# Kernel tuning notes

Measured on AMD Instinct MI355X. Metric: run time of the kernel, lower is better.

The kernel has to match this reference:

```python
import jax, jax.numpy as jnp
import numpy as np

H = 1024   # hidden_size
I = 2048   # intermediate_size
E = 16     # num_experts
K = 2      # num_experts_per_tok
B, T = 2, 2048


def setup_inputs() -> dict:
    key = jax.random.key(0)
    k1, k2, k3, k4 = jax.random.split(key, 4)
    x = jax.random.normal(k1, (B, T, H), dtype=jnp.float32)
    # torch nn.Linear weight layout: [out_features, in_features]
    Wg = jax.random.normal(k2, (E, H), dtype=jnp.float32) * 0.02   # gate
    W1 = jax.random.normal(k3, (E, I, H), dtype=jnp.float32) * 0.02  # fc1 per expert
    W2 = jax.random.normal(k4, (E, H, I), dtype=jnp.float32) * 0.02  # fc2 per expert
    return {"x": x, "Wg": Wg, "W1": W1, "W2": W2}


def reference(x, Wg, W1, W2):
    Bq, Tq, Hq = x.shape
    nt = Bq * Tq
    x_flat = x.reshape(nt, Hq)                       # [nt, H]
    gate_logits = x_flat @ Wg.T                      # [nt, E]
    gate_probs = jax.nn.softmax(gate_logits, axis=-1)
    topk_vals, topk_idx = jax.lax.top_k(gate_probs, K)  # [nt, K]
    # dense combine weights: zero for unselected (token, expert) pairs
    rows = jnp.arange(nt)[:, None]                   # [nt, 1]
    cw = jnp.zeros((nt, E), dtype=x.dtype).at[rows, topk_idx].add(topk_vals)
    # per-expert dense SiLU-MLP; combine weight of 0 makes unselected
    # contributions exactly zero, matching the original gather/scatter math.
    y_flat = jnp.zeros_like(x_flat)
    for e in range(E):
        h = jax.nn.silu(x_flat @ W1[e].T)            # [nt, I]
        o = h @ W2[e].T                              # [nt, H]
        y_flat = y_flat + cw[:, e:e + 1] * o
    return y_flat.reshape(Bq, Tq, Hq)
```

## Files before the change

kernel.cpp:

```cpp
#include <hip/hip_runtime.h>
#include <hip/hip_bf16.h>

#define H_DIM 1024
#define I_DIM 2048
#define NEXP  16
#define NTOK  4096
#define BM 128
#define BN 128
#define BK 32
#define ABUF (BM*BK)
#define BBUF (BN*BK)
#define MAXS 10240
#define MAXRB (MAXS/BM)
#define NC1 (I_DIM/BN)
#define NC2 (H_DIM/BN)
#define PAIRS (NTOK*2)
#define SORT_T 256
#define PPT (PAIRS/SORT_T)

typedef __attribute__((ext_vector_type(8))) short short8;
typedef __attribute__((ext_vector_type(4))) short short4v;
typedef __attribute__((ext_vector_type(4))) float f32x4;

#define OFF_TOKE 256
#define OFF_TOKW (OFF_TOKE + PAIRS*4)
#define OFF_TOS  (OFF_TOKW + PAIRS*4)
#define OFF_WOS  (OFF_TOS + MAXS*4)
#define OFF_H    (OFF_WOS + MAXS*4)
#define OFF_XBF  (OFF_H + (size_t)MAXS*I_DIM*2)
#define NEED_XBF (OFF_XBF + (size_t)NTOK*H_DIM*2)

#define GLDS16(gsrc, ldst) \
  __builtin_amdgcn_global_load_lds((const __attribute__((address_space(1))) void*)(gsrc), \
                                   (__attribute__((address_space(3))) void*)(ldst), 16, 0, 0)

__device__ inline short f2bf(float f) {
    union { float f; unsigned u; } v; v.f = f;
    unsigned u = v.u + 0x7FFFu + ((v.u >> 16) & 1u);
    return (short)(u >> 16);
}

__device__ inline short8 pack8(const float4 a, const float4 b) {
    return (short8){ f2bf(a.x), f2bf(a.y), f2bf(a.z), f2bf(a.w),
                     f2bf(b.x), f2bf(b.y), f2bf(b.z), f2bf(b.w) };
}

__device__ inline int xcd_swz(int bid, int nwg) {
    return (bid & 7) * (nwg >> 3) + (bid >> 3);
}

template<bool WRITE_XBF>
__global__ __launch_bounds__(256) void gate_kernel(
    const float* __restrict__ x, const float* __restrict__ Wg,
    int* __restrict__ tokE, float* __restrict__ tokW, short* __restrict__ xbf)
{
    const int tok  = blockIdx.x * 4 + (threadIdx.x >> 6);
    const int lane = threadIdx.x & 63;
    const float4* xr = (const float4*)(x + (size_t)tok * H_DIM);

    float acc[NEXP];
#pragma unroll
    for (int e = 0; e < NEXP; e++) acc[e] = 0.f;
#pragma unroll
    for (int j = 0; j < H_DIM/4; j += 64) {
        const float4 xv = xr[j + lane];
        if constexpr (WRITE_XBF) {
            *(short4v*)(xbf + (size_t)tok * H_DIM + (j + lane) * 4) =
                (short4v){ f2bf(xv.x), f2bf(xv.y), f2bf(xv.z), f2bf(xv.w) };
        }
#pragma unroll
        for (int e = 0; e < NEXP; e++) {
            const float4 wv = ((const float4*)(Wg + e * H_DIM))[j + lane];
            acc[e] = fmaf(xv.x, wv.x, fmaf(xv.y, wv.y, fmaf(xv.z, wv.z, fmaf(xv.w, wv.w, acc[e]))));
        }
    }
#pragma unroll
    for (int off = 32; off; off >>= 1) {
#pragma unroll
        for (int e = 0; e < NEXP; e++) acc[e] += __shfl_xor(acc[e], off, 64);
    }
    if (lane == 0) {
        float m = acc[0];
#pragma unroll
        for (int e = 1; e < NEXP; e++) m = fmaxf(m, acc[e]);
        float p[NEXP]; float s = 0.f;
#pragma unroll
        for (int e = 0; e < NEXP; e++) { p[e] = __expf(acc[e] - m); s += p[e]; }
        int i1 = 0;
#pragma unroll
        for (int e = 1; e < NEXP; e++) if (acc[e] > acc[i1]) i1 = e;
        int i2 = -1;
#pragma unroll
        for (int e = 0; e < NEXP; e++) {
            if (e == i1) continue;
            if (i2 < 0 || acc[e] > acc[i2]) i2 = e;
        }
        const float inv = 1.f / s;
        tokE[tok*2+0] = i1; tokW[tok*2+0] = p[i1] * inv;
        tokE[tok*2+1] = i2; tokW[tok*2+1] = p[i2] * inv;
    }
}

__global__ __launch_bounds__(SORT_T) void sort_kernel(
    const int* __restrict__ tokE, const float* __restrict__ tokW,
    int* __restrict__ aoff, int* __restrict__ tok_of_slot, float* __restrict__ w_of_slot)
{
    __shared__ int hist[NEXP * SORT_T];
    __shared__ int tot[NEXP];
    __shared__ int aoff_l[NEXP + 1];

    const int tid = threadIdx.x;
    const int lane = tid & 63, wv = tid >> 6;

    int eloc[PPT];
#pragma unroll
    for (int i = 0; i < PPT; i++) eloc[i] = tokE[tid * PPT + i];

#pragma unroll
    for (int e = 0; e < NEXP; e++) hist[e * SORT_T + tid] = 0;
    __syncthreads();
#pragma unroll
    for (int i = 0; i < PPT; i++) hist[eloc[i] * SORT_T + tid]++;
    __syncthreads();

#pragma unroll
    for (int r = 0; r < 4; r++) {
        const int e = wv * 4 + r;
        const int base = e * SORT_T + lane * 4;
        int v0 = hist[base+0], v1 = hist[base+1], v2 = hist[base+2], v3 = hist[base+3];
        const int s = v0 + v1 + v2 + v3;
        int incl = s;
#pragma unroll
        for (int off = 1; off < 64; off <<= 1) {
            const int t = __shfl_up(incl, off, 64);
            if (lane >= off) incl += t;
        }
        int run = incl - s;
        hist[base+0] = run; run += v0;
        hist[base+1] = run; run += v1;
        hist[base+2] = run; run += v2;
        hist[base+3] = run;
        if (lane == 63) tot[e] = incl;
    }
    __syncthreads();

    if (tid == 0) {
        int acc = 0;
#pragma unroll
        for (int e = 0; e < NEXP; e++) {
            aoff_l[e] = acc; aoff[e] = acc;
            acc += ((tot[e] + BM - 1) / BM) * BM;
        }
        aoff_l[NEXP] = acc; aoff[NEXP] = acc;
    }
    __syncthreads();

#pragma unroll
    for (int i = 0; i < PPT; i++) {
        const int p = tid * PPT + i;
        const int e = eloc[i];
        const int idx = hist[e * SORT_T + tid]++;
        const int slot = aoff_l[e] + idx;
        tok_of_slot[slot] = p >> 1;
        w_of_slot[slot] = tokW[p];
    }
}

template<int AMODE>
__global__ __launch_bounds__(256) void fc1_kernel_t(
    const void* __restrict__ xsrc, const float* __restrict__ W1,
    const int* __restrict__ aoff, const int* __restrict__ tok_of_slot,
    short* __restrict__ h)
{
    const int wg = xcd_swz(blockIdx.x, NC1 * MAXRB);
    const int colb = wg % NC1, rowb = wg / NC1;
    const int total = aoff[NEXP];
    const int row0 = rowb * BM;
    if (row0 >= total) return;
    int e = 0;
    while (aoff[e+1] <= row0) e++;
    const int col0 = colb * BN;

    __shared__ short As[2*ABUF];
    __shared__ short Bs[2*BBUF];

    const int tid = threadIdx.x, wid = tid>>6, lane = tid&63;
    const int wr = wid>>1, wc = wid&1;
    const int srow = wid*32 + (lane>>2);
    const int skc  = (lane&3)*8;

    int t0 = tok_of_slot[row0 + srow];      if (t0 < 0) t0 = 0;
    int t1 = tok_of_slot[row0 + srow + 16]; if (t1 < 0) t1 = 0;

    const float* wf0 = W1 + (size_t)e * I_DIM * H_DIM + (size_t)(col0 + srow)      * H_DIM + skc;
    const float* wf1 = W1 + (size_t)e * I_DIM * H_DIM + (size_t)(col0 + srow + 16) * H_DIM + skc;

    const short *sa0=nullptr,*sa1=nullptr;
    const float *fa0=nullptr,*fa1=nullptr;
    if constexpr (AMODE == 0) {
        const short* xb = (const short*)xsrc;
        sa0 = xb + (size_t)t0 * H_DIM + skc;
        sa1 = xb + (size_t)t1 * H_DIM + skc;
    } else {
        const float* xf = (const float*)xsrc;
        fa0 = xf + (size_t)t0 * H_DIM + skc;
        fa1 = xf + (size_t)t1 * H_DIM + skc;
    }
    short* la0 = &As[(wid*2+0)*512];
    short* la1 = &As[(wid*2+1)*512];

    const int frow = lane & 15, fko = (lane>>4)*8;

    f32x4 acc[4][4];
#pragma unroll
    for (int m=0;m<4;m++)
#pragma unroll
        for (int n=0;n<4;n++) acc[m][n] = (f32x4){0.f,0.f,0.f,0.f};

    float4 b00 = *(const float4*)(wf0), b01 = *(const float4*)(wf0+4);
    float4 b10 = *(const float4*)(wf1), b11 = *(const float4*)(wf1+4);
    float4 a00, a01, a10, a11;
    if constexpr (AMODE == 0) {
        GLDS16(sa0, la0);
        GLDS16(sa1, la1);
    } else {
        a00 = *(const float4*)(fa0); a01 = *(const float4*)(fa0+4);
        a10 = *(const float4*)(fa1); a11 = *(const float4*)(fa1+4);
        *(short8*)&As[srow*32 + skc]      = pack8(a00, a01);
        *(short8*)&As[(srow+16)*32 + skc] = pack8(a10, a11);
    }
    *(short8*)&Bs[srow*32 + skc]      = pack8(b00, b01);
    *(short8*)&Bs[(srow+16)*32 + skc] = pack8(b10, b11);
    __syncthreads();

    const int NT = H_DIM / BK;
    int cur = 0;
    for (int t = 0; t < NT; ++t) {
        const int kn = (t+1)*BK;
        const bool more = (t+1 < NT);
        if (more) {
            if constexpr (AMODE == 0) {
                GLDS16(sa0 + kn, la0 + (cur^1)*ABUF);
                GLDS16(sa1 + kn, la1 + (cur^1)*ABUF);
            } else {
                a00 = *(const float4*)(fa0+kn); a01 = *(const float4*)(fa0+kn+4);
                a10 = *(const float4*)(fa1+kn); a11 = *(const float4*)(fa1+kn+4);
            }
            b00 = *(const float4*)(wf0+kn); b01 = *(const float4*)(wf0+kn+4);
            b10 = *(const float4*)(wf1+kn); b11 = *(const float4*)(wf1+kn+4);
        }

        short8 af[4], bfr[4];
#pragma unroll
        for (int m=0;m<4;m++) af[m]  = *(const short8*)&As[cur*ABUF + (wr*64 + m*16 + frow)*32 + fko];
#pragma unroll
        for (int n=0;n<4;n++) bfr[n] = *(const short8*)&Bs[cur*BBUF + (wc*64 + n*16 + frow)*32 + fko];
#pragma unroll
        for (int m=0;m<4;m++)
#pragma unroll
            for (int n=0;n<4;n++)
                acc[m][n] = __builtin_amdgcn_mfma_f32_16x16x32_bf16(af[m], bfr[n], acc[m][n], 0, 0, 0);

        if (more) {
            if constexpr (AMODE == 1) {
                *(short8*)&As[(cur^1)*ABUF + srow*32 + skc]      = pack8(a00, a01);
                *(short8*)&As[(cur^1)*ABUF + (srow+16)*32 + skc] = pack8(a10, a11);
            }
            *(short8*)&Bs[(cur^1)*BBUF + srow*32 + skc]      = pack8(b00, b01);
            *(short8*)&Bs[(cur^1)*BBUF + (srow+16)*32 + skc] = pack8(b10, b11);
        }
        __syncthreads();
        cur ^= 1;
    }

    const int mr0 = row0 + wr*64 + (lane>>4)*4;
    const int nc0 = col0 + wc*64 + (lane&15);
#pragma unroll
    for (int m=0;m<4;m++)
#pragma unroll
        for (int n=0;n<4;n++)
#pragma unroll
            for (int r=0;r<4;r++) {
                const float v = acc[m][n][r];
                const float sv = v / (1.f + __expf(-v));
                h[(size_t)(mr0 + m*16 + r) * I_DIM + nc0 + n*16] = f2bf(sv);
            }
}

__global__ __launch_bounds__(256) void fc2_kernel(
    const short* __restrict__ h, const float* __restrict__ W2,
    const int* __restrict__ aoff, const int* __restrict__ tok_of_slot,
    const float* __restrict__ w_of_slot, float* __restrict__ y)
{
    const int wg = xcd_swz(blockIdx.x, NC2 * MAXRB);
    const int colb = wg % NC2, rowb = wg / NC2;
    const int total = aoff[NEXP];
    const int row0 = rowb * BM;
    if (row0 >= total) return;
    int e = 0;
    while (aoff[e+1] <= row0) e++;
    const int col0 = colb * BN;

    __shared__ short As[2*ABUF];
    __shared__ short Bs[2*BBUF];

    const int tid = threadIdx.x, wid = tid>>6, lane = tid&63;
    const int wr = wid>>1, wc = wid&1;
    const int srow = wid*32 + (lane>>2);
    const int skc  = (lane&3)*8;

    const short* sa0 = h + (size_t)(row0 + srow)      * I_DIM + skc;
    const short* sa1 = h + (size_t)(row0 + srow + 16) * I_DIM + skc;

    const float* wf0 = W2 + (size_t)e * H_DIM * I_DIM + (size_t)(col0 + srow)      * I_DIM + skc;
    const float* wf1 = W2 + (size_t)e * H_DIM * I_DIM + (size_t)(col0 + srow + 16) * I_DIM + skc;

    short* la0 = &As[(wid*2+0)*512];
    short* la1 = &As[(wid*2+1)*512];

    const int frow = lane & 15, fko = (lane>>4)*8;

    f32x4 acc[4][4];
#pragma unroll
    for (int m=0;m<4;m++)
#pragma unroll
        for (int n=0;n<4;n++) acc[m][n] = (f32x4){0.f,0.f,0.f,0.f};

    float4 b00 = *(const float4*)(wf0), b01 = *(const float4*)(wf0+4);
    float4 b10 = *(const float4*)(wf1), b11 = *(const float4*)(wf1+4);
    GLDS16(sa0, la0);
    GLDS16(sa1, la1);
    *(short8*)&Bs[srow*32 + skc]      = pack8(b00, b01);
    *(short8*)&Bs[(srow+16)*32 + skc] = pack8(b10, b11);
    __syncthreads();

    const int NT = I_DIM / BK;
    int cur = 0;
    for (int t = 0; t < NT; ++t) {
        const int kn = (t+1)*BK;
        const bool more = (t+1 < NT);
        if (more) {
            GLDS16(sa0 + kn, la0 + (cur^1)*ABUF);
            GLDS16(sa1 + kn, la1 + (cur^1)*ABUF);
            b00 = *(const float4*)(wf0+kn); b01 = *(const float4*)(wf0+kn+4);
            b10 = *(const float4*)(wf1+kn); b11 = *(const float4*)(wf1+kn+4);
        }

        short8 af[4], bfr[4];
#pragma unroll
        for (int m=0;m<4;m++) af[m]  = *(const short8*)&As[cur*ABUF + (wr*64 + m*16 + frow)*32 + fko];
#pragma unroll
        for (int n=0;n<4;n++) bfr[n] = *(const short8*)&Bs[cur*BBUF + (wc*64 + n*16 + frow)*32 + fko];
#pragma unroll
        for (int m=0;m<4;m++)
#pragma unroll
            for (int n=0;n<4;n++)
                acc[m][n] = __builtin_amdgcn_mfma_f32_16x16x32_bf16(af[m], bfr[n], acc[m][n], 0, 0, 0);

        if (more) {
            *(short8*)&Bs[(cur^1)*BBUF + srow*32 + skc]      = pack8(b00, b01);
            *(short8*)&Bs[(cur^1)*BBUF + (srow+16)*32 + skc] = pack8(b10, b11);
        }
        __syncthreads();
        cur ^= 1;
    }

    const int mr0 = row0 + wr*64 + (lane>>4)*4;
    const int nc0 = col0 + wc*64 + (lane&15);
#pragma unroll
    for (int m=0;m<4;m++)
#pragma unroll
        for (int r=0;r<4;r++) {
            const int slot = mr0 + m*16 + r;
            const int tok = tok_of_slot[slot];
            if (tok < 0) continue;
            const float w = w_of_slot[slot];
#pragma unroll
            for (int n=0;n<4;n++)
                atomicAdd(&y[(size_t)tok * H_DIM + nc0 + n*16], w * acc[m][n][r]);
        }
}

extern "C" void kernel_launch(void* const* d_in, const int* in_sizes, int n_in,
                              void* d_out, int out_size, void* d_ws, size_t ws_size,
                              hipStream_t stream) {
    const float* x  = (const float*)d_in[0];
    const float* Wg = (const float*)d_in[1];
    const float* W1 = (const float*)d_in[2];
    const float* W2 = (const float*)d_in[3];
    float* y = (float*)d_out;

    char* ws = (char*)d_ws;
    int*   aoff        = (int*)  (ws + 128);
    int*   tokE        = (int*)  (ws + OFF_TOKE);
    float* tokW        = (float*)(ws + OFF_TOKW);
    int*   tok_of_slot = (int*)  (ws + OFF_TOS);
    float* w_of_slot   = (float*)(ws + OFF_WOS);
    short* h           = (short*)(ws + OFF_H);
    short* xbf         = (short*)(ws + OFF_XBF);

    const bool hasXbf = (ws_size >= NEED_XBF);

    hipMemsetAsync(tok_of_slot, 0xFF, MAXS*4, stream);
    hipMemsetAsync(y, 0, (size_t)out_size * 4, stream);

    if (hasXbf) {
        gate_kernel<true><<<NTOK/4, 256, 0, stream>>>(x, Wg, tokE, tokW, xbf);
        sort_kernel<<<1, SORT_T, 0, stream>>>(tokE, tokW, aoff, tok_of_slot, w_of_slot);
        fc1_kernel_t<0><<<NC1*MAXRB, 256, 0, stream>>>(xbf, W1, aoff, tok_of_slot, h);
    } else {
        gate_kernel<false><<<NTOK/4, 256, 0, stream>>>(x, Wg, tokE, tokW, nullptr);
        sort_kernel<<<1, SORT_T, 0, stream>>>(tokE, tokW, aoff, tok_of_slot, w_of_slot);
        fc1_kernel_t<1><<<NC1*MAXRB, 256, 0, stream>>>(x, W1, aoff, tok_of_slot, h);
    }
    fc2_kernel<<<NC2*MAXRB, 256, 0, stream>>>(h, W2, aoff, tok_of_slot, w_of_slot, y);
}
```

Before: 261.8 us.

## Prefetch two K-tiles ahead in registers and barrier without waiting on vmem

Replaces direct global-to-LDS loads and the per-iteration __syncthreads with a register-staged pipeline in both expert GEMM kernels. Two register sets hold tiles t+1 and t+2, so global loads run two K-steps ahead. A custom barrier waits only on lgkmcnt and not on vmcnt, so outstanding global loads are not drained at each barrier. This costs more VGPRs for the double register staging, which could lower occupancy, and activations now pass through registers instead of the async LDS path.

Result: slower. 285.2 us (+8.9%).

```diff
diff --git a/kernel.cpp b/kernel.cpp
--- a/kernel.cpp
+++ b/kernel.cpp
@@ -30,10 +30,6 @@
 #define OFF_XBF  (OFF_H + (size_t)MAXS*I_DIM*2)
 #define NEED_XBF (OFF_XBF + (size_t)NTOK*H_DIM*2)
 
-#define GLDS16(gsrc, ldst) \
-  __builtin_amdgcn_global_load_lds((const __attribute__((address_space(1))) void*)(gsrc), \
-                                   (__attribute__((address_space(3))) void*)(ldst), 16, 0, 0)
-
 __device__ inline short f2bf(float f) {
     union { float f; unsigned u; } v; v.f = f;
     unsigned u = v.u + 0x7FFFu + ((v.u >> 16) & 1u);
@@ -48,6 +44,13 @@
 __device__ inline int xcd_swz(int bid, int nwg) {
     return (bid & 7) * (nwg >> 3) + (bid >> 3);
 }
+
+#define BARRIER_NOVM()                                     \
+    __builtin_amdgcn_sched_barrier(0);                     \
+    asm volatile("s_waitcnt lgkmcnt(0)" ::: "memory");     \
+    __builtin_amdgcn_sched_barrier(0);                     \
+    __builtin_amdgcn_s_barrier();                          \
+    __builtin_amdgcn_sched_barrier(0);
 
 template<bool WRITE_XBF>
 __global__ __launch_bounds__(256) void gate_kernel(
@@ -165,6 +168,12 @@
         w_of_slot[slot] = tokW[p];
     }
 }
+
+struct TileRegs {
+    short8 a0, a1;
+    float4 fa00, fa01, fa10, fa11;
+    float4 b00, b01, b10, b11;
+};
 
 template<int AMODE>
 __global__ __launch_bounds__(256) void fc1_kernel_t(
@@ -206,8 +215,6 @@
         fa0 = xf + (size_t)t0 * H_DIM + skc;
         fa1 = xf + (size_t)t1 * H_DIM + skc;
     }
-    short* la0 = &As[(wid*2+0)*512];
-    short* la1 = &As[(wid*2+1)*512];
 
     const int frow = lane & 15, fko = (lane>>4)*8;
 
@@ -217,60 +224,64 @@
 #pragma unroll
         for (int n=0;n<4;n++) acc[m][n] = (f32x4){0.f,0.f,0.f,0.f};
 
-    float4 b00 = *(const float4*)(wf0), b01 = *(const float4*)(wf0+4);
-    float4 b10 = *(const float4*)(wf1), b11 = *(const float4*)(wf1+4);
-    float4 a00, a01, a10, a11;
-    if constexpr (AMODE == 0) {
-        GLDS16(sa0, la0);
-        GLDS16(sa1, la1);
-    } else {
-        a00 = *(const float4*)(fa0); a01 = *(const float4*)(fa0+4);
-        a10 = *(const float4*)(fa1); a11 = *(const float4*)(fa1+4);
-        *(short8*)&As[srow*32 + skc]      = pack8(a00, a01);
-        *(short8*)&As[(srow+16)*32 + skc] = pack8(a10, a11);
-    }
-    *(short8*)&Bs[srow*32 + skc]      = pack8(b00, b01);
-    *(short8*)&Bs[(srow+16)*32 + skc] = pack8(b10, b11);
-    __syncthreads();
-
+#define P_LOAD(S, k)                                                          \
+    {                                                                         \
+        if constexpr (AMODE == 0) {                                           \
+            S.a0 = *(const short8*)(sa0 + (k));                               \
+            S.a1 = *(const short8*)(sa1 + (k));                               \
+        } else {                                                              \
+            S.fa00 = *(const float4*)(fa0 + (k)); S.fa01 = *(const float4*)(fa0 + (k) + 4); \
+            S.fa10 = *(const float4*)(fa1 + (k)); S.fa11 = *(const float4*)(fa1 + (k) + 4); \
+        }                                                                     \
+        S.b00 = *(const float4*)(wf0 + (k)); S.b01 = *(const float4*)(wf0 + (k) + 4); \
+        S.b10 = *(const float4*)(wf1 + (k)); S.b11 = *(const float4*)(wf1 + (k) + 4); \
+    }
+
+#define P_WRITE(S, buf)                                                       \
+    {                                                                         \
+        if constexpr (AMODE == 0) {                                           \
+            *(short8*)&As[(buf)*ABUF + srow*32 + skc]      = S.a0;            \
+            *(short8*)&As[(buf)*ABUF + (srow+16)*32 + skc] = S.a1;            \
+        } else {                                                              \
+            *(short8*)&As[(buf)*ABUF + srow*32 + skc]      = pack8(S.fa00, S.fa01); \
+            *(short8*)&As[(buf)*ABUF + (srow+16)*32 + skc] = pack8(S.fa10, S.fa11); \
+        }                                                                     \
+        *(short8*)&Bs[(buf)*BBUF + srow*32 + skc]      = pack8(S.b00, S.b01); \
+        *(short8*)&Bs[(buf)*BBUF + (srow+16)*32 + skc] = pack8(S.b10, S.b11); \
+    }
+
+#define P_MFMA(buf)                                                           \
+    {                                                                         \
+        short8 af[4], bfr[4];                                                 \
+        _Pragma("unroll")                                                     \
+        for (int m=0;m<4;m++) af[m]  = *(const short8*)&As[(buf)*ABUF + (wr*64 + m*16 + frow)*32 + fko]; \
+        _Pragma("unroll")                                                     \
+        for (int n=0;n<4;n++) bfr[n] = *(const short8*)&Bs[(buf)*BBUF + (wc*64 + n*16 + frow)*32 + fko]; \
+        _Pragma("unroll")                                                     \
+        for (int m=0;m<4;m++)                                                 \
+            _Pragma("unroll")                                                 \
+            for (int n=0;n<4;n++)                                             \
+                acc[m][n] = __builtin_amdgcn_mfma_f32_16x16x32_bf16(af[m], bfr[n], acc[m][n], 0, 0, 0); \
+    }
+
+    TileRegs s0, s1;
     const int NT = H_DIM / BK;
-    int cur = 0;
-    for (int t = 0; t < NT; ++t) {
-        const int kn = (t+1)*BK;
-        const bool more = (t+1 < NT);
-        if (more) {
-            if constexpr (AMODE == 0) {
-                GLDS16(sa0 + kn, la0 + (cur^1)*ABUF);
-                GLDS16(sa1 + kn, la1 + (cur^1)*ABUF);
-            } else {
-                a00 = *(const float4*)(fa0+kn); a01 = *(const float4*)(fa0+kn+4);
-                a10 = *(const float4*)(fa1+kn); a11 = *(const float4*)(fa1+kn+4);
-            }
-            b00 = *(const float4*)(wf0+kn); b01 = *(const float4*)(wf0+kn+4);
-            b10 = *(const float4*)(wf1+kn); b11 = *(const float4*)(wf1+kn+4);
-        }
-
-        short8 af[4], bfr[4];
-#pragma unroll
-        for (int m=0;m<4;m++) af[m]  = *(const short8*)&As[cur*ABUF + (wr*64 + m*16 + frow)*32 + fko];
-#pragma unroll
-        for (int n=0;n<4;n++) bfr[n] = *(const short8*)&Bs[cur*BBUF + (wc*64 + n*16 + frow)*32 + fko];
-#pragma unroll
-        for (int m=0;m<4;m++)
-#pragma unroll
-            for (int n=0;n<4;n++)
-                acc[m][n] = __builtin_amdgcn_mfma_f32_16x16x32_bf16(af[m], bfr[n], acc[m][n], 0, 0, 0);
-
-        if (more) {
-            if constexpr (AMODE == 1) {
-                *(short8*)&As[(cur^1)*ABUF + srow*32 + skc]      = pack8(a00, a01);
-                *(short8*)&As[(cur^1)*ABUF + (srow+16)*32 + skc] = pack8(a10, a11);
-            }
-            *(short8*)&Bs[(cur^1)*BBUF + srow*32 + skc]      = pack8(b00, b01);
-            *(short8*)&Bs[(cur^1)*BBUF + (srow+16)*32 + skc] = pack8(b10, b11);
-        }
-        __syncthreads();
-        cur ^= 1;
+
+    P_LOAD(s0, 0);
+    P_WRITE(s0, 0);
+    P_LOAD(s1, BK);
+    BARRIER_NOVM();
+
+    for (int t = 0; t < NT; t += 2) {
+        if (t + 2 < NT) { P_LOAD(s0, (t+2)*BK); }
+        P_MFMA(0);
+        if (t + 1 < NT) { P_WRITE(s1, 1); }
+        BARRIER_NOVM();
+
+        if (t + 3 < NT) { P_LOAD(s1, (t+3)*BK); }
+        P_MFMA(1);
+        if (t + 2 < NT) { P_WRITE(s0, 0); }
+        BARRIER_NOVM();
     }
 
     const int mr0 = row0 + wr*64 + (lane>>4)*4;
@@ -285,6 +296,9 @@
                 const float sv = v / (1.f + __expf(-v));
                 h[(size_t)(mr0 + m*16 + r) * I_DIM + nc0 + n*16] = f2bf(sv);
             }
+#undef P_LOAD
+#undef P_WRITE
+#undef P_MFMA
 }
 
 __global__ __launch_bounds__(256) void fc2_kernel(
@@ -315,9 +329,6 @@
     const float* wf0 = W2 + (size_t)e * H_DIM * I_DIM + (size_t)(col0 + srow)      * I_DIM + skc;
     const float* wf1 = W2 + (size_t)e * H_DIM * I_DIM + (size_t)(col0 + srow + 16) * I_DIM + skc;
 
-    short* la0 = &As[(wid*2+0)*512];
-    short* la1 = &As[(wid*2+1)*512];
-
     const int frow = lane & 15, fko = (lane>>4)*8;
 
     f32x4 acc[4][4];
@@ -326,43 +337,54 @@
 #pragma unroll
         for (int n=0;n<4;n++) acc[m][n] = (f32x4){0.f,0.f,0.f,0.f};
 
-    float4 b00 = *(const float4*)(wf0), b01 = *(const float4*)(wf0+4);
-    float4 b10 = *(const float4*)(wf1), b11 = *(const float4*)(wf1+4);
-    GLDS16(sa0, la0);
-    GLDS16(sa1, la1);
-    *(short8*)&Bs[srow*32 + skc]      = pack8(b00, b01);
-    *(short8*)&Bs[(srow+16)*32 + skc] = pack8(b10, b11);
-    __syncthreads();
-
+#define P_LOAD(S, k)                                                          \
+    {                                                                         \
+        S.a0 = *(const short8*)(sa0 + (k));                                   \
+        S.a1 = *(const short8*)(sa1 + (k));                                   \
+        S.b00 = *(const float4*)(wf0 + (k)); S.b01 = *(const float4*)(wf0 + (k) + 4); \
+        S.b10 = *(const float4*)(wf1 + (k)); S.b11 = *(const float4*)(wf1 + (k) + 4); \
+    }
+
+#define P_WRITE(S, buf)                                                       \
+    {                                                                         \
+        *(short8*)&As[(buf)*ABUF + srow*32 + skc]      = S.a0;                \
+        *(short8*)&As[(buf)*ABUF + (srow+16)*32 + skc] = S.a1;                \
+        *(short8*)&Bs[(buf)*BBUF + srow*32 + skc]      = pack8(S.b00, S.b01); \
+        *(short8*)&Bs[(buf)*BBUF + (srow+16)*32 + skc] = pack8(S.b10, S.b11); \
+    }
+
+#define P_MFMA(buf)                                                           \
+    {                                                                         \
+        short8 af[4], bfr[4];                                                 \
+        _Pragma("unroll")                                                     \
+        for (int m=0;m<4;m++) af[m]  = *(const short8*)&As[(buf)*ABUF + (wr*64 + m*16 + frow)*32 + fko]; \
+        _Pragma("unroll")                                                     \
+        for (int n=0;n<4;n++) bfr[n] = *(const short8*)&Bs[(buf)*BBUF + (wc*64 + n*16 + frow)*32 + fko]; \
+        _Pragma("unroll")                                                     \
+        for (int m=0;m<4;m++)                                                 \
+            _Pragma("unroll")                                                 \
+            for (int n=0;n<4;n++)                                             \
+                acc[m][n] = __builtin_amdgcn_mfma_f32_16x16x32_bf16(af[m], bfr[n], acc[m][n], 0, 0, 0); \
+    }
+
+    TileRegs s0, s1;
     const int NT = I_DIM / BK;
-    int cur = 0;
-    for (int t = 0; t < NT; ++t) {
-        const int kn = (t+1)*BK;
-        const bool more = (t+1 < NT);
-        if (more) {
-            GLDS16(sa0 + kn, la0 + (cur^1)*ABUF);
-            GLDS16(sa1 + kn, la1 + (cur^1)*ABUF);
-            b00 = *(const float4*)(wf0+kn); b01 = *(const float4*)(wf0+kn+4);
-            b10 = *(const float4*)(wf1+kn); b11 = *(const float4*)(wf1+kn+4);
-        }
-
-        short8 af[4], bfr[4];
-#pragma unroll
-        for (int m=0;m<4;m++) af[m]  = *(const short8*)&As[cur*ABUF + (wr*64 + m*16 + frow)*32 + fko];
-#pragma unroll
-        for (int n=0;n<4;n++) bfr[n] = *(const short8*)&Bs[cur*BBUF + (wc*64 + n*16 + frow)*32 + fko];
-#pragma unroll
-        for (int m=0;m<4;m++)
-#pragma unroll
-            for (int n=0;n<4;n++)
-                acc[m][n] = __builtin_amdgcn_mfma_f32_16x16x32_bf16(af[m], bfr[n], acc[m][n], 0, 0, 0);
-
-        if (more) {
-            *(short8*)&Bs[(cur^1)*BBUF + srow*32 + skc]      = pack8(b00, b01);
-            *(short8*)&Bs[(cur^1)*BBUF + (srow+16)*32 + skc] = pack8(b10, b11);
-        }
-        __syncthreads();
-        cur ^= 1;
+
+    P_LOAD(s0, 0);
+    P_WRITE(s0, 0);
+    P_LOAD(s1, BK);
+    BARRIER_NOVM();
+
+    for (int t = 0; t < NT; t += 2) {
+        if (t + 2 < NT) { P_LOAD(s0, (t+2)*BK); }
+        P_MFMA(0);
+        if (t + 1 < NT) { P_WRITE(s1, 1); }
+        BARRIER_NOVM();
+
+        if (t + 3 < NT) { P_LOAD(s1, (t+3)*BK); }
+        P_MFMA(1);
+        if (t + 2 < NT) { P_WRITE(s0, 0); }
+        BARRIER_NOVM();
     }
 
     const int mr0 = row0 + wr*64 + (lane>>4)*4;
@@ -379,6 +401,9 @@
             for (int n=0;n<4;n++)
                 atomicAdd(&y[(size_t)tok * H_DIM + nc0 + n*16], w * acc[m][n][r]);
         }
+#undef P_LOAD
+#undef P_WRITE
+#undef P_MFMA
 }
 
 extern "C" void kernel_launch(void* const* d_in, const int* in_sizes, int n_in,
```

## Pre-convert W2 to bf16 inside fc1 launch and load fc2 B tiles via LDS DMA

Applied to the files above, without the earlier changes.

When the workspace is large enough, every fc1 workgroup first runs a grid-stride loop that converts the full fp32 W2 tensor to bf16 in workspace. fc2 then streams bf16 W2 tiles straight into LDS with global_load_lds instead of loading fp32 and packing in registers. The fc2 main loop also drops double buffering for a single-buffer load/sync/compute/sync scheme. This halves fc2's weight read bytes and removes per-tile conversion, but adds a full W2 read and write pass each call and loses load/compute overlap in fc2.

New measurement: 264.7 us. Within noise of the previous version (+1.1%).

```diff
diff --git a/kernel.cpp b/kernel.cpp
--- a/kernel.cpp
+++ b/kernel.cpp
@@ -28,7 +28,9 @@
 #define OFF_WOS  (OFF_TOS + MAXS*4)
 #define OFF_H    (OFF_WOS + MAXS*4)
 #define OFF_XBF  (OFF_H + (size_t)MAXS*I_DIM*2)
-#define NEED_XBF (OFF_XBF + (size_t)NTOK*H_DIM*2)
+#define OFF_WBF  (OFF_XBF + (size_t)NTOK*H_DIM*2)
+#define NEED_XBF OFF_WBF
+#define NEED_FULL (OFF_WBF + (size_t)NEXP*I_DIM*H_DIM*2)
 
 #define GLDS16(gsrc, ldst) \
   __builtin_amdgcn_global_load_lds((const __attribute__((address_space(1))) void*)(gsrc), \
@@ -166,12 +168,23 @@
     }
 }
 
-template<int AMODE>
+template<int AMODE, bool CONVW2>
 __global__ __launch_bounds__(256) void fc1_kernel_t(
     const void* __restrict__ xsrc, const float* __restrict__ W1,
     const int* __restrict__ aoff, const int* __restrict__ tok_of_slot,
-    short* __restrict__ h)
+    short* __restrict__ h, const float* __restrict__ w2src, short* __restrict__ w2dst)
 {
+    if constexpr (CONVW2) {
+        const int n8 = NEXP*H_DIM*I_DIM/8;
+        int i = blockIdx.x * 256 + threadIdx.x;
+        const int stride = NC1*MAXRB*256;
+        for (; i < n8; i += stride) {
+            const float4 f0 = ((const float4*)w2src)[2*i];
+            const float4 f1 = ((const float4*)w2src)[2*i+1];
+            ((short8*)w2dst)[i] = pack8(f0, f1);
+        }
+    }
+
     const int wg = xcd_swz(blockIdx.x, NC1 * MAXRB);
     const int colb = wg % NC1, rowb = wg / NC1;
     const int total = aoff[NEXP];
@@ -287,8 +300,9 @@
             }
 }
 
-__global__ __launch_bounds__(256) void fc2_kernel(
-    const short* __restrict__ h, const float* __restrict__ W2,
+template<int MODE>
+__global__ __launch_bounds__(256) void fc2_kernel_t(
+    const short* __restrict__ h, const void* __restrict__ w2src,
     const int* __restrict__ aoff, const int* __restrict__ tok_of_slot,
     const float* __restrict__ w_of_slot, float* __restrict__ y)
 {
@@ -301,8 +315,8 @@
     while (aoff[e+1] <= row0) e++;
     const int col0 = colb * BN;
 
-    __shared__ short As[2*ABUF];
-    __shared__ short Bs[2*BBUF];
+    __shared__ short As[ABUF];
+    __shared__ short Bs[BBUF];
 
     const int tid = threadIdx.x, wid = tid>>6, lane = tid&63;
     const int wr = wid>>1, wc = wid&1;
@@ -312,11 +326,21 @@
     const short* sa0 = h + (size_t)(row0 + srow)      * I_DIM + skc;
     const short* sa1 = h + (size_t)(row0 + srow + 16) * I_DIM + skc;
 
-    const float* wf0 = W2 + (size_t)e * H_DIM * I_DIM + (size_t)(col0 + srow)      * I_DIM + skc;
-    const float* wf1 = W2 + (size_t)e * H_DIM * I_DIM + (size_t)(col0 + srow + 16) * I_DIM + skc;
-
+    const short *sb0=nullptr,*sb1=nullptr;
+    const float *fb0=nullptr,*fb1=nullptr;
+    if constexpr (MODE == 0) {
+        const short* wb = (const short*)w2src + (size_t)e * H_DIM * I_DIM;
+        sb0 = wb + (size_t)(col0 + srow)      * I_DIM + skc;
+        sb1 = wb + (size_t)(col0 + srow + 16) * I_DIM + skc;
+    } else {
+        const float* wf = (const float*)w2src + (size_t)e * H_DIM * I_DIM;
+        fb0 = wf + (size_t)(col0 + srow)      * I_DIM + skc;
+        fb1 = wf + (size_t)(col0 + srow + 16) * I_DIM + skc;
+    }
     short* la0 = &As[(wid*2+0)*512];
     short* la1 = &As[(wid*2+1)*512];
+    short* lb0 = &Bs[(wid*2+0)*512];
+    short* lb1 = &Bs[(wid*2+1)*512];
 
     const int frow = lane & 15, fko = (lane>>4)*8;
 
@@ -326,43 +350,31 @@
 #pragma unroll
         for (int n=0;n<4;n++) acc[m][n] = (f32x4){0.f,0.f,0.f,0.f};
 
-    float4 b00 = *(const float4*)(wf0), b01 = *(const float4*)(wf0+4);
-    float4 b10 = *(const float4*)(wf1), b11 = *(const float4*)(wf1+4);
-    GLDS16(sa0, la0);
-    GLDS16(sa1, la1);
-    *(short8*)&Bs[srow*32 + skc]      = pack8(b00, b01);
-    *(short8*)&Bs[(srow+16)*32 + skc] = pack8(b10, b11);
-    __syncthreads();
-
-    const int NT = I_DIM / BK;
-    int cur = 0;
-    for (int t = 0; t < NT; ++t) {
-        const int kn = (t+1)*BK;
-        const bool more = (t+1 < NT);
-        if (more) {
-            GLDS16(sa0 + kn, la0 + (cur^1)*ABUF);
-            GLDS16(sa1 + kn, la1 + (cur^1)*ABUF);
-            b00 = *(const float4*)(wf0+kn); b01 = *(const float4*)(wf0+kn+4);
-            b10 = *(const float4*)(wf1+kn); b11 = *(const float4*)(wf1+kn+4);
-        }
+    for (int k0 = 0; k0 < I_DIM; k0 += BK) {
+        GLDS16(sa0 + k0, la0);
+        GLDS16(sa1 + k0, la1);
+        if constexpr (MODE == 0) {
+            GLDS16(sb0 + k0, lb0);
+            GLDS16(sb1 + k0, lb1);
+        } else {
+            const float4 b00 = *(const float4*)(fb0 + k0), b01 = *(const float4*)(fb0 + k0 + 4);
+            const float4 b10 = *(const float4*)(fb1 + k0), b11 = *(const float4*)(fb1 + k0 + 4);
+            *(short8*)&Bs[srow*32 + skc]      = pack8(b00, b01);
+            *(short8*)&Bs[(srow+16)*32 + skc] = pack8(b10, b11);
+        }
+        __syncthreads();
 
         short8 af[4], bfr[4];
 #pragma unroll
-        for (int m=0;m<4;m++) af[m]  = *(const short8*)&As[cur*ABUF + (wr*64 + m*16 + frow)*32 + fko];
-#pragma unroll
-        for (int n=0;n<4;n++) bfr[n] = *(const short8*)&Bs[cur*BBUF + (wc*64 + n*16 + frow)*32 + fko];
+        for (int m=0;m<4;m++) af[m]  = *(const short8*)&As[(wr*64 + m*16 + frow)*32 + fko];
+#pragma unroll
+        for (int n=0;n<4;n++) bfr[n] = *(const short8*)&Bs[(wc*64 + n*16 + frow)*32 + fko];
 #pragma unroll
         for (int m=0;m<4;m++)
 #pragma unroll
             for (int n=0;n<4;n++)
                 acc[m][n] = __builtin_amdgcn_mfma_f32_16x16x32_bf16(af[m], bfr[n], acc[m][n], 0, 0, 0);
-
-        if (more) {
-            *(short8*)&Bs[(cur^1)*BBUF + srow*32 + skc]      = pack8(b00, b01);
-            *(short8*)&Bs[(cur^1)*BBUF + (srow+16)*32 + skc] = pack8(b10, b11);
-        }
         __syncthreads();
-        cur ^= 1;
     }
 
     const int mr0 = row0 + wr*64 + (lane>>4)*4;
@@ -398,20 +410,28 @@
     float* w_of_slot   = (float*)(ws + OFF_WOS);
     short* h           = (short*)(ws + OFF_H);
     short* xbf         = (short*)(ws + OFF_XBF);
-
+    short* wbf         = (short*)(ws + OFF_WBF);
+
+    const bool full   = (ws_size >= NEED_FULL);
     const bool hasXbf = (ws_size >= NEED_XBF);
 
     hipMemsetAsync(tok_of_slot, 0xFF, MAXS*4, stream);
     hipMemsetAsync(y, 0, (size_t)out_size * 4, stream);
 
-    if (hasXbf) {
+    if (full) {
         gate_kernel<true><<<NTOK/4, 256, 0, stream>>>(x, Wg, tokE, tokW, xbf);
         sort_kernel<<<1, SORT_T, 0, stream>>>(tokE, tokW, aoff, tok_of_slot, w_of_slot);
-        fc1_kernel_t<0><<<NC1*MAXRB, 256, 0, stream>>>(xbf, W1, aoff, tok_of_slot, h);
+        fc1_kernel_t<0, true><<<NC1*MAXRB, 256, 0, stream>>>(xbf, W1, aoff, tok_of_slot, h, W2, wbf);
+        fc2_kernel_t<0><<<NC2*MAXRB, 256, 0, stream>>>(h, wbf, aoff, tok_of_slot, w_of_slot, y);
+    } else if (hasXbf) {
+        gate_kernel<true><<<NTOK/4, 256, 0, stream>>>(x, Wg, tokE, tokW, xbf);
+        sort_kernel<<<1, SORT_T, 0, stream>>>(tokE, tokW, aoff, tok_of_slot, w_of_slot);
+        fc1_kernel_t<0, false><<<NC1*MAXRB, 256, 0, stream>>>(xbf, W1, aoff, tok_of_slot, h, nullptr, nullptr);
+        fc2_kernel_t<1><<<NC2*MAXRB, 256, 0, stream>>>(h, W2, aoff, tok_of_slot, w_of_slot, y);
     } else {
         gate_kernel<false><<<NTOK/4, 256, 0, stream>>>(x, Wg, tokE, tokW, nullptr);
         sort_kernel<<<1, SORT_T, 0, stream>>>(tokE, tokW, aoff, tok_of_slot, w_of_slot);
-        fc1_kernel_t<1><<<NC1*MAXRB, 256, 0, stream>>>(x, W1, aoff, tok_of_slot, h);
-    }
-    fc2_kernel<<<NC2*MAXRB, 256, 0, stream>>>(h, W2, aoff, tok_of_slot, w_of_slot, y);
-}
+        fc1_kernel_t<1, false><<<NC1*MAXRB, 256, 0, stream>>>(x, W1, aoff, tok_of_slot, h, nullptr, nullptr);
+        fc2_kernel_t<1><<<NC2*MAXRB, 256, 0, stream>>>(h, W2, aoff, tok_of_slot, w_of_slot, y);
+    }
+}
```

## Stage fp32 weights into LDS via direct loads with XOR swizzle, convert at fragment read

Applied to the files above, without the earlier changes.

Both expert GEMM kernels now copy the fp32 weight tiles straight from global memory into LDS with global_load_lds, using an XOR-swizzled column layout. Each thread converts to bf16 with v_cvt_pk_bf16_f32 when it reads its MFMA fragment, so the register staging and software f2bf packing of the B operand go away. The double-buffered pipeline is replaced by a single buffer with a sync before and after compute, so load latency is no longer overlapped with MFMA work. The B tile in LDS doubles in size because it is held as fp32.

After: 264.6 us. No clear change (+1.1%).

```diff
diff --git a/kernel.cpp b/kernel.cpp
--- a/kernel.cpp
+++ b/kernel.cpp
@@ -9,7 +9,7 @@
 #define BN 128
 #define BK 32
 #define ABUF (BM*BK)
-#define BBUF (BN*BK)
+#define BFL  (BN*BK)
 #define MAXS 10240
 #define MAXRB (MAXS/BM)
 #define NC1 (I_DIM/BN)
@@ -47,6 +47,19 @@
 
 __device__ inline int xcd_swz(int bid, int nwg) {
     return (bid & 7) * (nwg >> 3) + (bid >> 3);
+}
+
+__device__ inline short8 ldB(const float* Bs, int row, int l16) {
+    const int s  = (row & 7) * 16;
+    const char* base = (const char*)(Bs + row * 32);
+    const f32x4 lo = *(const f32x4*)(base + (((l16 * 32)      ) ^ s));
+    const f32x4 hi = *(const f32x4*)(base + (((l16 * 32) + 16 ) ^ s));
+    union { unsigned u[4]; short8 sv; } pk;
+    asm("v_cvt_pk_bf16_f32 %0, %1, %2" : "=v"(pk.u[0]) : "v"(lo[0]), "v"(lo[1]));
+    asm("v_cvt_pk_bf16_f32 %0, %1, %2" : "=v"(pk.u[1]) : "v"(lo[2]), "v"(lo[3]));
+    asm("v_cvt_pk_bf16_f32 %0, %1, %2" : "=v"(pk.u[2]) : "v"(hi[0]), "v"(hi[1]));
+    asm("v_cvt_pk_bf16_f32 %0, %1, %2" : "=v"(pk.u[3]) : "v"(hi[2]), "v"(hi[3]));
+    return pk.sv;
 }
 
 template<bool WRITE_XBF>
@@ -181,8 +194,8 @@
     while (aoff[e+1] <= row0) e++;
     const int col0 = colb * BN;
 
-    __shared__ short As[2*ABUF];
-    __shared__ short Bs[2*BBUF];
+    __shared__ short As[ABUF];
+    __shared__ __align__(16) float Bs[BFL];
 
     const int tid = threadIdx.x, wid = tid>>6, lane = tid&63;
     const int wr = wid>>1, wc = wid&1;
@@ -191,9 +204,6 @@
 
     int t0 = tok_of_slot[row0 + srow];      if (t0 < 0) t0 = 0;
     int t1 = tok_of_slot[row0 + srow + 16]; if (t1 < 0) t1 = 0;
-
-    const float* wf0 = W1 + (size_t)e * I_DIM * H_DIM + (size_t)(col0 + srow)      * H_DIM + skc;
-    const float* wf1 = W1 + (size_t)e * I_DIM * H_DIM + (size_t)(col0 + srow + 16) * H_DIM + skc;
 
     const short *sa0=nullptr,*sa1=nullptr;
     const float *fa0=nullptr,*fa1=nullptr;
@@ -209,7 +219,19 @@
     short* la0 = &As[(wid*2+0)*512];
     short* la1 = &As[(wid*2+1)*512];
 
-    const int frow = lane & 15, fko = (lane>>4)*8;
+    const float* Wb = W1 + (size_t)e * I_DIM * H_DIM;
+    const int br  = lane >> 3;
+    const int bco = ((lane & 7) ^ br) * 4;
+    const float* bs0 = Wb + (size_t)(col0 + (wid*4+0)*8 + br) * H_DIM + bco;
+    const float* bs1 = Wb + (size_t)(col0 + (wid*4+1)*8 + br) * H_DIM + bco;
+    const float* bs2 = Wb + (size_t)(col0 + (wid*4+2)*8 + br) * H_DIM + bco;
+    const float* bs3 = Wb + (size_t)(col0 + (wid*4+3)*8 + br) * H_DIM + bco;
+    float* lb0 = &Bs[(wid*4+0)*256];
+    float* lb1 = &Bs[(wid*4+1)*256];
+    float* lb2 = &Bs[(wid*4+2)*256];
+    float* lb3 = &Bs[(wid*4+3)*256];
+
+    const int frow = lane & 15, fko = (lane>>4)*8, l16 = lane>>4;
 
     f32x4 acc[4][4];
 #pragma unroll
@@ -217,60 +239,33 @@
 #pragma unroll
         for (int n=0;n<4;n++) acc[m][n] = (f32x4){0.f,0.f,0.f,0.f};
 
-    float4 b00 = *(const float4*)(wf0), b01 = *(const float4*)(wf0+4);
-    float4 b10 = *(const float4*)(wf1), b11 = *(const float4*)(wf1+4);
-    float4 a00, a01, a10, a11;
-    if constexpr (AMODE == 0) {
-        GLDS16(sa0, la0);
-        GLDS16(sa1, la1);
-    } else {
-        a00 = *(const float4*)(fa0); a01 = *(const float4*)(fa0+4);
-        a10 = *(const float4*)(fa1); a11 = *(const float4*)(fa1+4);
-        *(short8*)&As[srow*32 + skc]      = pack8(a00, a01);
-        *(short8*)&As[(srow+16)*32 + skc] = pack8(a10, a11);
-    }
-    *(short8*)&Bs[srow*32 + skc]      = pack8(b00, b01);
-    *(short8*)&Bs[(srow+16)*32 + skc] = pack8(b10, b11);
-    __syncthreads();
-
-    const int NT = H_DIM / BK;
-    int cur = 0;
-    for (int t = 0; t < NT; ++t) {
-        const int kn = (t+1)*BK;
-        const bool more = (t+1 < NT);
-        if (more) {
-            if constexpr (AMODE == 0) {
-                GLDS16(sa0 + kn, la0 + (cur^1)*ABUF);
-                GLDS16(sa1 + kn, la1 + (cur^1)*ABUF);
-            } else {
-                a00 = *(const float4*)(fa0+kn); a01 = *(const float4*)(fa0+kn+4);
-                a10 = *(const float4*)(fa1+kn); a11 = *(const float4*)(fa1+kn+4);
-            }
-            b00 = *(const float4*)(wf0+kn); b01 = *(const float4*)(wf0+kn+4);
-            b10 = *(const float4*)(wf1+kn); b11 = *(const float4*)(wf1+kn+4);
-        }
+    for (int k0 = 0; k0 < H_DIM; k0 += BK) {
+        if constexpr (AMODE == 0) {
+            GLDS16(sa0 + k0, la0);
+            GLDS16(sa1 + k0, la1);
+        } else {
+            const float4 a00 = *(const float4*)(fa0+k0), a01 = *(const float4*)(fa0+k0+4);
+            const float4 a10 = *(const float4*)(fa1+k0), a11 = *(const float4*)(fa1+k0+4);
+            *(short8*)&As[srow*32 + skc]      = pack8(a00, a01);
+            *(short8*)&As[(srow+16)*32 + skc] = pack8(a10, a11);
+        }
+        GLDS16(bs0 + k0, lb0);
+        GLDS16(bs1 + k0, lb1);
+        GLDS16(bs2 + k0, lb2);
+        GLDS16(bs3 + k0, lb3);
+        __syncthreads();
 
         short8 af[4], bfr[4];
 #pragma unroll
-        for (int m=0;m<4;m++) af[m]  = *(const short8*)&As[cur*ABUF + (wr*64 + m*16 + frow)*32 + fko];
-#pragma unroll
-        for (int n=0;n<4;n++) bfr[n] = *(const short8*)&Bs[cur*BBUF + (wc*64 + n*16 + frow)*32 + fko];
+        for (int m=0;m<4;m++) af[m]  = *(const short8*)&As[(wr*64 + m*16 + frow)*32 + fko];
+#pragma unroll
+        for (int n=0;n<4;n++) bfr[n] = ldB(Bs, wc*64 + n*16 + frow, l16);
 #pragma unroll
         for (int m=0;m<4;m++)
 #pragma unroll
             for (int n=0;n<4;n++)
                 acc[m][n] = __builtin_amdgcn_mfma_f32_16x16x32_bf16(af[m], bfr[n], acc[m][n], 0, 0, 0);
-
-        if (more) {
-            if constexpr (AMODE == 1) {
-                *(short8*)&As[(cur^1)*ABUF + srow*32 + skc]      = pack8(a00, a01);
-                *(short8*)&As[(cur^1)*ABUF + (srow+16)*32 + skc] = pack8(a10, a11);
-            }
-            *(short8*)&Bs[(cur^1)*BBUF + srow*32 + skc]      = pack8(b00, b01);
-            *(short8*)&Bs[(cur^1)*BBUF + (srow+16)*32 + skc] = pack8(b10, b11);
-        }
         __syncthreads();
-        cur ^= 1;
     }
 
     const int mr0 = row0 + wr*64 + (lane>>4)*4;
@@ -301,8 +296,8 @@
     while (aoff[e+1] <= row0) e++;
     const int col0 = colb * BN;
 
-    __shared__ short As[2*ABUF];
-    __shared__ short Bs[2*BBUF];
+    __shared__ short As[ABUF];
+    __shared__ __align__(16) float Bs[BFL];
 
     const int tid = threadIdx.x, wid = tid>>6, lane = tid&63;
     const int wr = wid>>1, wc = wid&1;
@@ -311,14 +306,22 @@
 
     const short* sa0 = h + (size_t)(row0 + srow)      * I_DIM + skc;
     const short* sa1 = h + (size_t)(row0 + srow + 16) * I_DIM + skc;
-
-    const float* wf0 = W2 + (size_t)e * H_DIM * I_DIM + (size_t)(col0 + srow)      * I_DIM + skc;
-    const float* wf1 = W2 + (size_t)e * H_DIM * I_DIM + (size_t)(col0 + srow + 16) * I_DIM + skc;
-
     short* la0 = &As[(wid*2+0)*512];
     short* la1 = &As[(wid*2+1)*512];
 
-    const int frow = lane & 15, fko = (lane>>4)*8;
+    const float* Wb = W2 + (size_t)e * H_DIM * I_DIM;
+    const int br  = lane >> 3;
+    const int bco = ((lane & 7) ^ br) * 4;
+    const float* bs0 = Wb + (size_t)(col0 + (wid*4+0)*8 + br) * I_DIM + bco;
+    const float* bs1 = Wb + (size_t)(col0 + (wid*4+1)*8 + br) * I_DIM + bco;
+    const float* bs2 = Wb + (size_t)(col0 + (wid*4+2)*8 + br) * I_DIM + bco;
+    const float* bs3 = Wb + (size_t)(col0 + (wid*4+3)*8 + br) * I_DIM + bco;
+    float* lb0 = &Bs[(wid*4+0)*256];
+    float* lb1 = &Bs[(wid*4+1)*256];
+    float* lb2 = &Bs[(wid*4+2)*256];
+    float* lb3 = &Bs[(wid*4+3)*256];
+
+    const int frow = lane & 15, fko = (lane>>4)*8, l16 = lane>>4;
 
     f32x4 acc[4][4];
 #pragma unroll
@@ -326,43 +329,26 @@
 #pragma unroll
         for (int n=0;n<4;n++) acc[m][n] = (f32x4){0.f,0.f,0.f,0.f};
 
-    float4 b00 = *(const float4*)(wf0), b01 = *(const float4*)(wf0+4);
-    float4 b10 = *(const float4*)(wf1), b11 = *(const float4*)(wf1+4);
-    GLDS16(sa0, la0);
-    GLDS16(sa1, la1);
-    *(short8*)&Bs[srow*32 + skc]      = pack8(b00, b01);
-    *(short8*)&Bs[(srow+16)*32 + skc] = pack8(b10, b11);
-    __syncthreads();
-
-    const int NT = I_DIM / BK;
-    int cur = 0;
-    for (int t = 0; t < NT; ++t) {
-        const int kn = (t+1)*BK;
-        const bool more = (t+1 < NT);
-        if (more) {
-            GLDS16(sa0 + kn, la0 + (cur^1)*ABUF);
-            GLDS16(sa1 + kn, la1 + (cur^1)*ABUF);
-            b00 = *(const float4*)(wf0+kn); b01 = *(const float4*)(wf0+kn+4);
-            b10 = *(const float4*)(wf1+kn); b11 = *(const float4*)(wf1+kn+4);
-        }
+    for (int k0 = 0; k0 < I_DIM; k0 += BK) {
+        GLDS16(sa0 + k0, la0);
+        GLDS16(sa1 + k0, la1);
+        GLDS16(bs0 + k0, lb0);
+        GLDS16(bs1 + k0, lb1);
+        GLDS16(bs2 + k0, lb2);
+        GLDS16(bs3 + k0, lb3);
+        __syncthreads();
 
         short8 af[4], bfr[4];
 #pragma unroll
-        for (int m=0;m<4;m++) af[m]  = *(const short8*)&As[cur*ABUF + (wr*64 + m*16 + frow)*32 + fko];
-#pragma unroll
-        for (int n=0;n<4;n++) bfr[n] = *(const short8*)&Bs[cur*BBUF + (wc*64 + n*16 + frow)*32 + fko];
+        for (int m=0;m<4;m++) af[m]  = *(const short8*)&As[(wr*64 + m*16 + frow)*32 + fko];
+#pragma unroll
+        for (int n=0;n<4;n++) bfr[n] = ldB(Bs, wc*64 + n*16 + frow, l16);
 #pragma unroll
         for (int m=0;m<4;m++)
 #pragma unroll
             for (int n=0;n<4;n++)
                 acc[m][n] = __builtin_amdgcn_mfma_f32_16x16x32_bf16(af[m], bfr[n], acc[m][n], 0, 0, 0);
-
-        if (more) {
-            *(short8*)&Bs[(cur^1)*BBUF + srow*32 + skc]      = pack8(b00, b01);
-            *(short8*)&Bs[(cur^1)*BBUF + (srow+16)*32 + skc] = pack8(b10, b11);
-        }
         __syncthreads();
-        cur ^= 1;
     }
 
     const int mr0 = row0 + wr*64 + (lane>>4)*4;
```
